# Kernel tuning notes

Hardware: AMD Instinct MI355X
Metric: run time of the kernel (lower is better)

Reference implementation:

```python
import jax, jax.numpy as jnp
import numpy as np

# Hyperparameters matching init_kwargs
IN_CH = 64
OUT_CH = 128
KERNEL = (3, 3)
STRIDE = (1, 1)
PADDING = 'SAME'
K_ORDER = 3          # spline order
G_INTERVALS = 3      # grid intervals
GRID_MIN, GRID_MAX = -1.0, 1.0
N_BASIS = G_INTERVALS + K_ORDER  # basis functions per input = 6
PATCH_DIM = IN_CH * KERNEL[0] * KERNEL[1]  # 576


def _grid():
    # Extended uniform knot vector: G + 2k + 1 knots
    h = (GRID_MAX - GRID_MIN) / G_INTERVALS
    return jnp.arange(-K_ORDER, G_INTERVALS + K_ORDER + 1, dtype=jnp.float32) * h + GRID_MIN


def _b_splines(x):
    # x: [N, n_in] -> bases: [N, n_in, G + k]
    grid = _grid()  # [G + 2k + 1]
    xe = x[..., None]  # [N, n_in, 1]
    bases = ((xe >= grid[:-1]) & (xe < grid[1:])).astype(x.dtype)  # order-0, [N, n_in, G+2k]
    for p in range(1, K_ORDER + 1):
        left = (xe - grid[: -(p + 1)]) / (grid[p:-1] - grid[: -(p + 1)]) * bases[..., :-1]
        right = (grid[p + 1:] - xe) / (grid[p + 1:] - grid[1:-p]) * bases[..., 1:]
        bases = left + right
    return bases  # [N, n_in, G + k]


def setup_inputs() -> dict:
    key = jax.random.key(0)
    k0, k1, k2, k3 = jax.random.split(key, 4)
    x = jax.random.normal(k0, (8, 64, 64, IN_CH), dtype=jnp.float32)
    base_w = jax.random.normal(k1, (OUT_CH, PATCH_DIM), dtype=jnp.float32) * 0.05
    spline_w = jax.random.normal(k2, (OUT_CH, PATCH_DIM, N_BASIS), dtype=jnp.float32) * 0.05
    bias = jax.random.normal(k3, (OUT_CH,), dtype=jnp.float32) * 0.05
    return {'x': x, 'base_w': base_w, 'spline_w': spline_w, 'bias': bias}


def reference(x, base_w, spline_w, bias):
    batch = x.shape[0]
    dn = ('NHWC', 'HWIO', 'NHWC')
    patches = jax.lax.conv_general_dilated_patches(
        lhs=x, filter_shape=KERNEL, window_strides=STRIDE, padding=PADDING,
        dimension_numbers=dn)  # [B, H, W, patch_dim]
    out_spatial = patches.shape[1:-1]
    p = patches.reshape(-1, PATCH_DIM)  # [N, patch_dim]
    # EfficientKAN: residual (silu) branch + spline branch + bias
    base_out = jax.nn.silu(p) @ base_w.T                      # [N, out]
    bases = _b_splines(p)                                      # [N, patch_dim, G+k]
    spline_out = jnp.einsum('nig,oig->no', bases, spline_w)    # [N, out]
    y = base_out + spline_out + bias
    return y.reshape(batch, *out_spatial, OUT_CH)
```

## Files before the change

kernel.cpp:

```cpp
#include <hip/hip_runtime.h>

typedef __attribute__((ext_vector_type(8))) short short8;
typedef __attribute__((ext_vector_type(16))) float f32x16;

#define FT2_SHORTS (512u * 4356u * 8u)
#define PLANE16    4356

typedef __attribute__((address_space(3))) unsigned int lds_u32_t;
typedef __attribute__((address_space(1))) const unsigned int g_u32_t;

__device__ __forceinline__ unsigned short f2bf(float x) {
    union { float f; unsigned u; } v; v.f = x;
    unsigned r = v.u + 0x7FFFu + ((v.u >> 16) & 1u);
    return (unsigned short)(r >> 16);
}

__device__ __forceinline__ void feat8(float p, unsigned short* uf) {
    float e   = __expf(-p);
    float sig = 1.f / (1.f + e);
    uf[0] = f2bf(p * sig);
    float u  = p * 1.5f + 4.5f;
    float fj = floorf(u);
    int   j0 = (int)fj;
    float t  = u - fj;
    bool  inr = (u >= 0.f) && (u < 9.f);
    float t2 = t * t, t3 = t2 * t;
    const float c16 = 1.f / 6.f;
    float r0 = t3 * c16;
    float r1 = (-3.f * t3 + 3.f * t2 + 3.f * t + 1.f) * c16;
    float r2 = (3.f * t3 - 6.f * t2 + 4.f) * c16;
    float s1 = 1.f - t;
    float r3 = s1 * s1 * s1 * c16;
#pragma unroll
    for (int g = 0; g < 6; ++g) {
        int r = j0 - g;
        float v = (r == 0) ? r0 : ((r == 1) ? r1 : ((r == 2) ? r2 : ((r == 3) ? r3 : 0.f)));
        uf[1 + g] = f2bf(inr ? v : 0.f);
    }
    uf[7] = 0;
}

__global__ __launch_bounds__(256)
void prep_all(const float* __restrict__ x,
              const float* __restrict__ bw, const float* __restrict__ sw,
              unsigned short* __restrict__ ft, unsigned short* __restrict__ wt) {
    const int blk = blockIdx.x;
    const int tid = threadIdx.x;

    if (tid < 144) {
        int idx = blk * 144 + tid;
        int o = idx / 576;
        int i = idx - o * 576;
        int slab = i >> 3, e = i & 7;
        union { unsigned short u[8]; uint4 v; } pk;
        pk.u[0] = f2bf(bw[o * 576 + i]);
        const float* s = sw + (size_t)(o * 576 + i) * 6;
#pragma unroll
        for (int f = 0; f < 6; ++f) pk.u[1 + f] = f2bf(s[f]);
        pk.u[7] = 0;
        *(uint4*)(wt + ((size_t)slab * 8192 + e * 1024 + o * 8)) = pk.v;
    }

    {
        short8 pad = { 0, 0, (short)0x3CAB, (short)0x3EF5,
                       (short)0x3EF5, (short)0x3CAB, 0, 0 };
        for (int t = tid; t < 260; t += 256) {
            int yy, xx;
            if (t < 66)       { yy = 0;       xx = t; }
            else if (t < 132) { yy = 65;      xx = t - 66; }
            else if (t < 196) { yy = t - 131; xx = 0; }
            else              { yy = t - 195; xx = 65; }
            ((short8*)ft)[blk * PLANE16 + yy * 66 + xx] = pad;
        }
    }

    __shared__ float Xl[64 * 65];
    const int b = blk >> 6, y = blk & 63;
    const float* xl = x + (size_t)blk * 4096;
    for (int f4 = tid; f4 < 1024; f4 += 256) {
        float4 v = ((const float4*)xl)[f4];
        int xx = f4 >> 4, c4 = (f4 & 15) << 2;
        float* d = &Xl[xx * 65 + c4];
        d[0] = v.x; d[1] = v.y; d[2] = v.z; d[3] = v.w;
    }
    __syncthreads();
    const int xx = tid & 63;
    const int cw = tid >> 6;
#pragma unroll 4
    for (int p = 0; p < 16; ++p) {
        int c = cw + (p << 2);
        float pv = Xl[xx * 65 + c];
        union { unsigned short u[8]; uint4 v; } pk;
        feat8(pv, pk.u);
        size_t o16 = (size_t)(c * 8 + b) * PLANE16 + (y + 1) * 66 + (xx + 1);
        *(uint4*)(ft + (o16 << 3)) = pk.v;
    }
}

#define BUF_SHORTS 16384

#define STAGE(sl, q_)                                                                 \
    {                                                                                 \
        unsigned short* bufq = Bufs + (q_) * BUF_SHORTS;                              \
        const unsigned short* bsrc = wt + (size_t)(sl) * 8192;                        \
        _Pragma("unroll")                                                             \
        for (int t = 0; t < 2; ++t) {                                                 \
            int u = wave * 2 + t;                     \
            if (u < 16) {                                                             \
                int boff = u * 512 + lane * 8;                                        \
                __builtin_amdgcn_global_load_lds((g_u32_t*)(bsrc + boff),             \
                                                 (lds_u32_t*)(bufq + boff), 16, 0, 0);\
            } else {                                                                  \
                int ua  = u - 16;                                 \
                int ia  = (sl) * 8 + (ua >> 1);                                       \
                int ln  = ua & 1;                                                     \
                int c_  = (ia * 7282) >> 16;                                          \
                int i9_ = ia - c_ * 9;                                                \
                int kh_ = (i9_ * 11) >> 5;                                            \
                int kw_ = i9_ - kh_ * 3;                                              \
                const unsigned short* asrc = ft +                                     \
                    (((size_t)(c_ * 8 + b) * PLANE16 + (y0 + ln + kh_) * 66 + kw_)    \
                     << 3) + lane * 8;                                                \
                unsigned short* adst = bufq + 8192 + ua * 512 + lane * 8;             \
                __builtin_amdgcn_global_load_lds((g_u32_t*)asrc, (lds_u32_t*)adst,    \
                                                 16, 0, 0);                           \
            }                                                                         \
        }                                                                             \
    }

#define COMPUTE(q_)                                                                   \
    {                                                                                 \
        const unsigned short* bufr = Bufs + (q_) * BUF_SHORTS;                        \
        const unsigned short* Ab = bufr + 8192 + ((iloc << 1) + mh) * 512;            \
        const unsigned short* Bb = bufr + iloc * 1024 + nh * 512;                     \
        short8 a0 = *(const short8*)(Ab + l32 * 8);                                   \
        short8 a1 = *(const short8*)(Ab + 256 + l32 * 8);                             \
        short8 b0 = *(const short8*)(Bb + l32 * 8);                                   \
        short8 b1 = *(const short8*)(Bb + 256 + l32 * 8);                             \
        acc00 = __builtin_amdgcn_mfma_f32_32x32x16_bf16(a0, b0, acc00, 0, 0, 0);      \
        acc01 = __builtin_amdgcn_mfma_f32_32x32x16_bf16(a0, b1, acc01, 0, 0, 0);      \
        acc10 = __builtin_amdgcn_mfma_f32_32x32x16_bf16(a1, b0, acc10, 0, 0, 0);      \
        acc11 = __builtin_amdgcn_mfma_f32_32x32x16_bf16(a1, b1, acc11, 0, 0, 0);      \
    }

#define PHASE(q_, n_, stagesl, dostage_)                                              \
    {                                                                                 \
        asm volatile("s_waitcnt vmcnt(" #n_ ")" ::: "memory");                        \
        __builtin_amdgcn_s_barrier();                                                 \
        asm volatile("" ::: "memory");                                                \
        __builtin_amdgcn_s_setprio(1);                                                \
        COMPUTE(q_)                                                                   \
        __builtin_amdgcn_s_setprio(0);                                                \
        asm volatile("" ::: "memory");                                                \
        __builtin_amdgcn_s_barrier();                                                 \
        asm volatile("" ::: "memory");                                                \
        if (dostage_) STAGE(stagesl, q_);                                             \
    }

#define DUMPA(base_, A_)                                                              \
    {   float4* s4 = (float4*)(red + (base_));                                        \
        _Pragma("unroll")                                                             \
        for (int c = 0; c < 4; ++c)                                                   \
            s4[c * 64 + lane] = make_float4(A_[4*c], A_[4*c+1], A_[4*c+2], A_[4*c+3]); }
#define ADDA(base_, A_)                                                               \
    {   const float4* s4 = (const float4*)(red + (base_));                            \
        _Pragma("unroll")                                                             \
        for (int c = 0; c < 4; ++c) {                                                 \
            float4 rv = s4[c * 64 + lane];                                            \
            A_[4*c] += rv.x; A_[4*c+1] += rv.y; A_[4*c+2] += rv.z; A_[4*c+3] += rv.w; } }

__global__ __launch_bounds__(1024, 4)
void convkan_gemm(const unsigned short* __restrict__ ft,
                  const unsigned short* __restrict__ wt,
                  const float* __restrict__ bias,
                  float* __restrict__ out) {
    extern __shared__ unsigned short Bufs[];

    const int tid  = threadIdx.x;
    const int mb   = blockIdx.x;
    const int lane = tid & 63;
    const int wave = tid >> 6;
    const int kq   = wave >> 2;
    const int mh   = (wave >> 1) & 1;
    const int nh   = wave & 1;
    const int l32  = lane & 31;
    const int h    = lane >> 5;
    const int iloc = (kq << 1) + h;

    const int b  = mb >> 5;
    const int y0 = (mb & 31) << 1;

    f32x16 acc00, acc01, acc10, acc11;
#pragma unroll
    for (int e = 0; e < 16; ++e) { acc00[e] = 0.f; acc01[e] = 0.f; acc10[e] = 0.f; acc11[e] = 0.f; }

    STAGE(0, 0);
    STAGE(1, 1);
    STAGE(2, 2);

    for (int it3 = 0; it3 < 23; ++it3) {
        const int it = it3 * 3;
        PHASE(0, 4, it + 3, true)
        PHASE(1, 4, it + 4, true)
        PHASE(2, 4, it + 5, true)
    }
    PHASE(0, 4, 0, false)
    PHASE(1, 2, 0, false)
    PHASE(2, 0, 0, false)

    __syncthreads();
    float* red = (float*)Bufs;
    const int grp = mh * 2 + nh;

    if (kq >= 2) { DUMPA(((grp << 1) + (kq - 2)) * 2048,        acc00);
                   DUMPA(((grp << 1) + (kq - 2)) * 2048 + 1024, acc01); }
    __syncthreads();
    if (kq < 2)  { ADDA(((grp << 1) + kq) * 2048,        acc00);
                   ADDA(((grp << 1) + kq) * 2048 + 1024, acc01); }
    __syncthreads();
    if (kq >= 2) { DUMPA(((grp << 1) + (kq - 2)) * 2048,        acc10);
                   DUMPA(((grp << 1) + (kq - 2)) * 2048 + 1024, acc11); }
    __syncthreads();
    if (kq < 2)  { ADDA(((grp << 1) + kq) * 2048,        acc10);
                   ADDA(((grp << 1) + kq) * 2048 + 1024, acc11); }
    __syncthreads();
    if (kq == 1) { DUMPA(grp * 4096,        acc00); DUMPA(grp * 4096 + 1024, acc01);
                   DUMPA(grp * 4096 + 2048, acc10); DUMPA(grp * 4096 + 3072, acc11); }
    __syncthreads();
    if (kq == 0) {
        ADDA(grp * 4096,        acc00); ADDA(grp * 4096 + 1024, acc01);
        ADDA(grp * 4096 + 2048, acc10); ADDA(grp * 4096 + 3072, acc11);

        const int ncol = nh * 64 + l32;
        const float bv0 = bias[ncol];
        const float bv1 = bias[ncol + 32];
        const int prow = mb * 128 + mh * 64;
#pragma unroll
        for (int r = 0; r < 16; ++r) {
            int mrow = (r & 3) + ((r >> 2) << 3) + 4 * h;
            float* p = out + (size_t)(prow + mrow) * 128 + ncol;
            p[0]  = acc00[r] + bv0;
            p[32] = acc01[r] + bv1;
            float* p2 = out + (size_t)(prow + 32 + mrow) * 128 + ncol;
            p2[0]  = acc10[r] + bv0;
            p2[32] = acc11[r] + bv1;
        }
    }
}

extern "C" void kernel_launch(void* const* d_in, const int* in_sizes, int n_in,
                              void* d_out, int out_size, void* d_ws, size_t ws_size,
                              hipStream_t stream) {
    (void)in_sizes; (void)n_in; (void)ws_size; (void)out_size;
    const float* x        = (const float*)d_in[0];
    const float* base_w   = (const float*)d_in[1];
    const float* spline_w = (const float*)d_in[2];
    const float* bias     = (const float*)d_in[3];
    float* out = (float*)d_out;

    unsigned short* ft = (unsigned short*)d_ws;
    unsigned short* wt = ft + FT2_SHORTS;

    hipLaunchKernelGGL(prep_all, dim3(512), dim3(256), 0, stream,
                       x, base_w, spline_w, ft, wt);

    const int shmem = 3 * BUF_SHORTS * 2;
    (void)hipFuncSetAttribute((const void*)convkan_gemm,
                              hipFuncAttributeMaxDynamicSharedMemorySize, shmem);
    hipLaunchKernelGGL(convkan_gemm, dim3(256), dim3(1024), shmem, stream,
                       ft, wt, bias, out);
}
```

Baseline: 133.4 us.

## Halve GEMM block tile to one output row and double grid with swizzled block order

```diff
diff --git a/kernel.cpp b/kernel.cpp
--- a/kernel.cpp
+++ b/kernel.cpp
@@ -97,31 +97,30 @@
     }
 }
 
-#define BUF_SHORTS 16384
+#define BUF_SHORTS 12288
 
 #define STAGE(sl, q_)                                                                 \
     {                                                                                 \
         unsigned short* bufq = Bufs + (q_) * BUF_SHORTS;                              \
         const unsigned short* bsrc = wt + (size_t)(sl) * 8192;                        \
         _Pragma("unroll")                                                             \
-        for (int t = 0; t < 2; ++t) {                                                 \
-            int u = wave * 2 + t;                     \
+        for (int t = 0; t < 3; ++t) {                                                 \
+            int u = wave * 3 + t;                     \
             if (u < 16) {                                                             \
                 int boff = u * 512 + lane * 8;                                        \
                 __builtin_amdgcn_global_load_lds((g_u32_t*)(bsrc + boff),             \
                                                  (lds_u32_t*)(bufq + boff), 16, 0, 0);\
             } else {                                                                  \
-                int ua  = u - 16;                                 \
-                int ia  = (sl) * 8 + (ua >> 1);                                       \
-                int ln  = ua & 1;                                                     \
+                int idx = u - 16;                                     \
+                int ia  = (sl) * 8 + idx;                                             \
                 int c_  = (ia * 7282) >> 16;                                          \
                 int i9_ = ia - c_ * 9;                                                \
                 int kh_ = (i9_ * 11) >> 5;                                            \
                 int kw_ = i9_ - kh_ * 3;                                              \
                 const unsigned short* asrc = ft +                                     \
-                    (((size_t)(c_ * 8 + b) * PLANE16 + (y0 + ln + kh_) * 66 + kw_)    \
-                     << 3) + lane * 8;                                                \
-                unsigned short* adst = bufq + 8192 + ua * 512 + lane * 8;             \
+                    (((size_t)(c_ * 8 + b) * PLANE16 + (y + kh_) * 66 + kw_) << 3)    \
+                    + lane * 8;                                                       \
+                unsigned short* adst = bufq + 8192 + idx * 512 + lane * 8;            \
                 __builtin_amdgcn_global_load_lds((g_u32_t*)asrc, (lds_u32_t*)adst,    \
                                                  16, 0, 0);                           \
             }                                                                         \
@@ -131,10 +130,10 @@
 #define COMPUTE(q_)                                                                   \
     {                                                                                 \
         const unsigned short* bufr = Bufs + (q_) * BUF_SHORTS;                        \
-        const unsigned short* Ab = bufr + 8192 + ((iloc << 1) + mh) * 512;            \
+        const unsigned short* Ab = bufr + 8192 + iloc * 512;                          \
         const unsigned short* Bb = bufr + iloc * 1024 + nh * 512;                     \
         short8 a0 = *(const short8*)(Ab + l32 * 8);                                   \
-        short8 a1 = *(const short8*)(Ab + 256 + l32 * 8);                             \
+        short8 a1 = *(const short8*)(Ab + (32 + l32) * 8);                            \
         short8 b0 = *(const short8*)(Bb + l32 * 8);                                   \
         short8 b1 = *(const short8*)(Bb + 256 + l32 * 8);                             \
         acc00 = __builtin_amdgcn_mfma_f32_32x32x16_bf16(a0, b0, acc00, 0, 0, 0);      \
@@ -169,7 +168,7 @@
             float4 rv = s4[c * 64 + lane];                                            \
             A_[4*c] += rv.x; A_[4*c+1] += rv.y; A_[4*c+2] += rv.z; A_[4*c+3] += rv.w; } }
 
-__global__ __launch_bounds__(1024, 4)
+__global__ __launch_bounds__(512, 4)
 void convkan_gemm(const unsigned short* __restrict__ ft,
                   const unsigned short* __restrict__ wt,
                   const float* __restrict__ bias,
@@ -177,18 +176,18 @@
     extern __shared__ unsigned short Bufs[];
 
     const int tid  = threadIdx.x;
-    const int mb   = blockIdx.x;
+    const int blk  = blockIdx.x;
+    const int mb   = ((blk & 7) << 6) | (blk >> 3);
     const int lane = tid & 63;
     const int wave = tid >> 6;
-    const int kq   = wave >> 2;
-    const int mh   = (wave >> 1) & 1;
+    const int kq   = wave >> 1;
     const int nh   = wave & 1;
     const int l32  = lane & 31;
     const int h    = lane >> 5;
     const int iloc = (kq << 1) + h;
 
-    const int b  = mb >> 5;
-    const int y0 = (mb & 31) << 1;
+    const int b = mb >> 6;
+    const int y = mb & 63;
 
     f32x16 acc00, acc01, acc10, acc11;
 #pragma unroll
@@ -200,41 +199,40 @@
 
     for (int it3 = 0; it3 < 23; ++it3) {
         const int it = it3 * 3;
-        PHASE(0, 4, it + 3, true)
-        PHASE(1, 4, it + 4, true)
-        PHASE(2, 4, it + 5, true)
-    }
-    PHASE(0, 4, 0, false)
-    PHASE(1, 2, 0, false)
+        PHASE(0, 6, it + 3, true)
+        PHASE(1, 6, it + 4, true)
+        PHASE(2, 6, it + 5, true)
+    }
+    PHASE(0, 6, 0, false)
+    PHASE(1, 3, 0, false)
     PHASE(2, 0, 0, false)
 
     __syncthreads();
     float* red = (float*)Bufs;
-    const int grp = mh * 2 + nh;
-
-    if (kq >= 2) { DUMPA(((grp << 1) + (kq - 2)) * 2048,        acc00);
-                   DUMPA(((grp << 1) + (kq - 2)) * 2048 + 1024, acc01); }
-    __syncthreads();
-    if (kq < 2)  { ADDA(((grp << 1) + kq) * 2048,        acc00);
-                   ADDA(((grp << 1) + kq) * 2048 + 1024, acc01); }
-    __syncthreads();
-    if (kq >= 2) { DUMPA(((grp << 1) + (kq - 2)) * 2048,        acc10);
-                   DUMPA(((grp << 1) + (kq - 2)) * 2048 + 1024, acc11); }
-    __syncthreads();
-    if (kq < 2)  { ADDA(((grp << 1) + kq) * 2048,        acc10);
-                   ADDA(((grp << 1) + kq) * 2048 + 1024, acc11); }
-    __syncthreads();
-    if (kq == 1) { DUMPA(grp * 4096,        acc00); DUMPA(grp * 4096 + 1024, acc01);
-                   DUMPA(grp * 4096 + 2048, acc10); DUMPA(grp * 4096 + 3072, acc11); }
+
+    if (kq >= 2) { DUMPA(((nh << 1) + (kq - 2)) * 2048,        acc00);
+                   DUMPA(((nh << 1) + (kq - 2)) * 2048 + 1024, acc01); }
+    __syncthreads();
+    if (kq < 2)  { ADDA(((nh << 1) + kq) * 2048,        acc00);
+                   ADDA(((nh << 1) + kq) * 2048 + 1024, acc01); }
+    __syncthreads();
+    if (kq >= 2) { DUMPA(((nh << 1) + (kq - 2)) * 2048,        acc10);
+                   DUMPA(((nh << 1) + (kq - 2)) * 2048 + 1024, acc11); }
+    __syncthreads();
+    if (kq < 2)  { ADDA(((nh << 1) + kq) * 2048,        acc10);
+                   ADDA(((nh << 1) + kq) * 2048 + 1024, acc11); }
+    __syncthreads();
+    if (kq == 1) { DUMPA(nh * 4096,        acc00); DUMPA(nh * 4096 + 1024, acc01);
+                   DUMPA(nh * 4096 + 2048, acc10); DUMPA(nh * 4096 + 3072, acc11); }
     __syncthreads();
     if (kq == 0) {
-        ADDA(grp * 4096,        acc00); ADDA(grp * 4096 + 1024, acc01);
-        ADDA(grp * 4096 + 2048, acc10); ADDA(grp * 4096 + 3072, acc11);
+        ADDA(nh * 4096,        acc00); ADDA(nh * 4096 + 1024, acc01);
+        ADDA(nh * 4096 + 2048, acc10); ADDA(nh * 4096 + 3072, acc11);
 
         const int ncol = nh * 64 + l32;
         const float bv0 = bias[ncol];
         const float bv1 = bias[ncol + 32];
-        const int prow = mb * 128 + mh * 64;
+        const int prow = mb * 64;
 #pragma unroll
         for (int r = 0; r < 16; ++r) {
             int mrow = (r & 3) + ((r >> 2) << 3) + 4 * h;
@@ -267,6 +265,6 @@
     const int shmem = 3 * BUF_SHORTS * 2;
     (void)hipFuncSetAttribute((const void*)convkan_gemm,
                               hipFuncAttributeMaxDynamicSharedMemorySize, shmem);
-    hipLaunchKernelGGL(convkan_gemm, dim3(256), dim3(1024), shmem, stream,
+    hipLaunchKernelGGL(convkan_gemm, dim3(512), dim3(512), shmem, stream,
                        ft, wt, bias, out);
 }
```

New measurement: 135.7 us. About the same (+1.8%).

## Split K across two blocks with atomic accumulation and swizzled block order

Applied to the files above, without the earlier changes.

```diff
diff --git a/kernel.cpp b/kernel.cpp
--- a/kernel.cpp
+++ b/kernel.cpp
@@ -97,22 +97,22 @@
     }
 }
 
-#define BUF_SHORTS 16384
-
-#define STAGE(sl, q_)                                                                 \
+#define BUF_SHORTS 8192
+
+#define STAGE(hs, q_)                                                                 \
     {                                                                                 \
         unsigned short* bufq = Bufs + (q_) * BUF_SHORTS;                              \
-        const unsigned short* bsrc = wt + (size_t)(sl) * 8192;                        \
+        const unsigned short* bsrc = wt + (size_t)(kk72 + (hs)) * 4096;               \
         _Pragma("unroll")                                                             \
         for (int t = 0; t < 2; ++t) {                                                 \
-            int u = wave * 2 + t;                     \
-            if (u < 16) {                                                             \
+            int u = wave * 2 + t;                       \
+            if (u < 8) {                                                              \
                 int boff = u * 512 + lane * 8;                                        \
                 __builtin_amdgcn_global_load_lds((g_u32_t*)(bsrc + boff),             \
                                                  (lds_u32_t*)(bufq + boff), 16, 0, 0);\
             } else {                                                                  \
-                int ua  = u - 16;                                 \
-                int ia  = (sl) * 8 + (ua >> 1);                                       \
+                int ua  = u - 8;                              \
+                int ia  = (kk72 + (hs)) * 4 + (ua >> 1);                              \
                 int ln  = ua & 1;                                                     \
                 int c_  = (ia * 7282) >> 16;                                          \
                 int i9_ = ia - c_ * 9;                                                \
@@ -121,7 +121,7 @@
                 const unsigned short* asrc = ft +                                     \
                     (((size_t)(c_ * 8 + b) * PLANE16 + (y0 + ln + kh_) * 66 + kw_)    \
                      << 3) + lane * 8;                                                \
-                unsigned short* adst = bufq + 8192 + ua * 512 + lane * 8;             \
+                unsigned short* adst = bufq + 4096 + ua * 512 + lane * 8;             \
                 __builtin_amdgcn_global_load_lds((g_u32_t*)asrc, (lds_u32_t*)adst,    \
                                                  16, 0, 0);                           \
             }                                                                         \
@@ -131,19 +131,17 @@
 #define COMPUTE(q_)                                                                   \
     {                                                                                 \
         const unsigned short* bufr = Bufs + (q_) * BUF_SHORTS;                        \
-        const unsigned short* Ab = bufr + 8192 + ((iloc << 1) + mh) * 512;            \
-        const unsigned short* Bb = bufr + iloc * 1024 + nh * 512;                     \
-        short8 a0 = *(const short8*)(Ab + l32 * 8);                                   \
-        short8 a1 = *(const short8*)(Ab + 256 + l32 * 8);                             \
-        short8 b0 = *(const short8*)(Bb + l32 * 8);                                   \
-        short8 b1 = *(const short8*)(Bb + 256 + l32 * 8);                             \
+        short8 a0 = *(const short8*)(bufr + aoff);                                    \
+        short8 a1 = *(const short8*)(bufr + aoff + 256);                              \
+        short8 b0 = *(const short8*)(bufr + boff);                                    \
+        short8 b1 = *(const short8*)(bufr + boff + 256);                              \
         acc00 = __builtin_amdgcn_mfma_f32_32x32x16_bf16(a0, b0, acc00, 0, 0, 0);      \
         acc01 = __builtin_amdgcn_mfma_f32_32x32x16_bf16(a0, b1, acc01, 0, 0, 0);      \
         acc10 = __builtin_amdgcn_mfma_f32_32x32x16_bf16(a1, b0, acc10, 0, 0, 0);      \
         acc11 = __builtin_amdgcn_mfma_f32_32x32x16_bf16(a1, b1, acc11, 0, 0, 0);      \
     }
 
-#define PHASE(q_, n_, stagesl, dostage_)                                              \
+#define PHASE(q_, n_, stagehs, dostage_)                                              \
     {                                                                                 \
         asm volatile("s_waitcnt vmcnt(" #n_ ")" ::: "memory");                        \
         __builtin_amdgcn_s_barrier();                                                 \
@@ -154,7 +152,7 @@
         asm volatile("" ::: "memory");                                                \
         __builtin_amdgcn_s_barrier();                                                 \
         asm volatile("" ::: "memory");                                                \
-        if (dostage_) STAGE(stagesl, q_);                                             \
+        if (dostage_) STAGE(stagehs, q_);                                             \
     }
 
 #define DUMPA(base_, A_)                                                              \
@@ -169,7 +167,7 @@
             float4 rv = s4[c * 64 + lane];                                            \
             A_[4*c] += rv.x; A_[4*c+1] += rv.y; A_[4*c+2] += rv.z; A_[4*c+3] += rv.w; } }
 
-__global__ __launch_bounds__(1024, 4)
+__global__ __launch_bounds__(512, 4)
 void convkan_gemm(const unsigned short* __restrict__ ft,
                   const unsigned short* __restrict__ wt,
                   const float* __restrict__ bias,
@@ -177,7 +175,10 @@
     extern __shared__ unsigned short Bufs[];
 
     const int tid  = threadIdx.x;
-    const int mb   = blockIdx.x;
+    const int blk  = blockIdx.x;
+    const int kk   = blk >> 8;
+    const int mbr  = blk & 255;
+    const int mb   = ((mbr & 7) << 5) | (mbr >> 3);
     const int lane = tid & 63;
     const int wave = tid >> 6;
     const int kq   = wave >> 2;
@@ -185,10 +186,14 @@
     const int nh   = wave & 1;
     const int l32  = lane & 31;
     const int h    = lane >> 5;
-    const int iloc = (kq << 1) + h;
 
     const int b  = mb >> 5;
     const int y0 = (mb & 31) << 1;
+    const int kk72 = kk * 72;
+
+    const int eloc = (kq << 1) + h;
+    const int aoff = 4096 + eloc * 1024 + mh * 512 + l32 * 8;
+    const int boff = eloc * 1024 + nh * 512 + l32 * 8;
 
     f32x16 acc00, acc01, acc10, acc11;
 #pragma unroll
@@ -212,38 +217,32 @@
     float* red = (float*)Bufs;
     const int grp = mh * 2 + nh;
 
-    if (kq >= 2) { DUMPA(((grp << 1) + (kq - 2)) * 2048,        acc00);
-                   DUMPA(((grp << 1) + (kq - 2)) * 2048 + 1024, acc01); }
-    __syncthreads();
-    if (kq < 2)  { ADDA(((grp << 1) + kq) * 2048,        acc00);
-                   ADDA(((grp << 1) + kq) * 2048 + 1024, acc01); }
-    __syncthreads();
-    if (kq >= 2) { DUMPA(((grp << 1) + (kq - 2)) * 2048,        acc10);
-                   DUMPA(((grp << 1) + (kq - 2)) * 2048 + 1024, acc11); }
-    __syncthreads();
-    if (kq < 2)  { ADDA(((grp << 1) + kq) * 2048,        acc10);
-                   ADDA(((grp << 1) + kq) * 2048 + 1024, acc11); }
-    __syncthreads();
-    if (kq == 1) { DUMPA(grp * 4096,        acc00); DUMPA(grp * 4096 + 1024, acc01);
-                   DUMPA(grp * 4096 + 2048, acc10); DUMPA(grp * 4096 + 3072, acc11); }
+    if (kq == 1) { DUMPA(grp * 2048,        acc00);
+                   DUMPA(grp * 2048 + 1024, acc01); }
+    __syncthreads();
+    if (kq == 0) { ADDA(grp * 2048,        acc00);
+                   ADDA(grp * 2048 + 1024, acc01); }
+    __syncthreads();
+    if (kq == 1) { DUMPA(grp * 2048,        acc10);
+                   DUMPA(grp * 2048 + 1024, acc11); }
     __syncthreads();
     if (kq == 0) {
-        ADDA(grp * 4096,        acc00); ADDA(grp * 4096 + 1024, acc01);
-        ADDA(grp * 4096 + 2048, acc10); ADDA(grp * 4096 + 3072, acc11);
+        ADDA(grp * 2048,        acc10);
+        ADDA(grp * 2048 + 1024, acc11);
 
         const int ncol = nh * 64 + l32;
-        const float bv0 = bias[ncol];
-        const float bv1 = bias[ncol + 32];
+        const float bv0 = kk ? 0.f : bias[ncol];
+        const float bv1 = kk ? 0.f : bias[ncol + 32];
         const int prow = mb * 128 + mh * 64;
 #pragma unroll
         for (int r = 0; r < 16; ++r) {
             int mrow = (r & 3) + ((r >> 2) << 3) + 4 * h;
             float* p = out + (size_t)(prow + mrow) * 128 + ncol;
-            p[0]  = acc00[r] + bv0;
-            p[32] = acc01[r] + bv1;
+            atomicAdd(p,      acc00[r] + bv0);
+            atomicAdd(p + 32, acc01[r] + bv1);
             float* p2 = out + (size_t)(prow + 32 + mrow) * 128 + ncol;
-            p2[0]  = acc10[r] + bv0;
-            p2[32] = acc11[r] + bv1;
+            atomicAdd(p2,      acc10[r] + bv0);
+            atomicAdd(p2 + 32, acc11[r] + bv1);
         }
     }
 }
@@ -251,7 +250,7 @@
 extern "C" void kernel_launch(void* const* d_in, const int* in_sizes, int n_in,
                               void* d_out, int out_size, void* d_ws, size_t ws_size,
                               hipStream_t stream) {
-    (void)in_sizes; (void)n_in; (void)ws_size; (void)out_size;
+    (void)in_sizes; (void)n_in; (void)ws_size;
     const float* x        = (const float*)d_in[0];
     const float* base_w   = (const float*)d_in[1];
     const float* spline_w = (const float*)d_in[2];
@@ -261,12 +260,13 @@
     unsigned short* ft = (unsigned short*)d_ws;
     unsigned short* wt = ft + FT2_SHORTS;
 
+    hipMemsetAsync(out, 0, (size_t)out_size * sizeof(float), stream);
     hipLaunchKernelGGL(prep_all, dim3(512), dim3(256), 0, stream,
                        x, base_w, spline_w, ft, wt);
 
     const int shmem = 3 * BUF_SHORTS * 2;
     (void)hipFuncSetAttribute((const void*)convkan_gemm,
                               hipFuncAttributeMaxDynamicSharedMemorySize, shmem);
-    hipLaunchKernelGGL(convkan_gemm, dim3(256), dim3(1024), shmem, stream,
+    hipLaunchKernelGGL(convkan_gemm, dim3(512), dim3(512), shmem, stream,
                        ft, wt, bias, out);
 }
```

Measured after the change: 150.5 us. 1.13x slower.

## Load GEMM operands directly from global into registers, dropping LDS staging

Applied to the files above, without the earlier changes.

```diff
diff --git a/kernel.cpp b/kernel.cpp
--- a/kernel.cpp
+++ b/kernel.cpp
@@ -5,9 +5,6 @@
 
 #define FT2_SHORTS (512u * 4356u * 8u)
 #define PLANE16    4356
-
-typedef __attribute__((address_space(3))) unsigned int lds_u32_t;
-typedef __attribute__((address_space(1))) const unsigned int g_u32_t;
 
 __device__ __forceinline__ unsigned short f2bf(float x) {
     union { float f; unsigned u; } v; v.f = x;
@@ -51,14 +48,13 @@
         int idx = blk * 144 + tid;
         int o = idx / 576;
         int i = idx - o * 576;
-        int slab = i >> 3, e = i & 7;
         union { unsigned short u[8]; uint4 v; } pk;
         pk.u[0] = f2bf(bw[o * 576 + i]);
         const float* s = sw + (size_t)(o * 576 + i) * 6;
 #pragma unroll
         for (int f = 0; f < 6; ++f) pk.u[1 + f] = f2bf(s[f]);
         pk.u[7] = 0;
-        *(uint4*)(wt + ((size_t)slab * 8192 + e * 1024 + o * 8)) = pk.v;
+        *(uint4*)(wt + ((size_t)i * 1024 + o * 8)) = pk.v;
     }
 
     {
@@ -97,64 +93,38 @@
     }
 }
 
-#define BUF_SHORTS 16384
-
-#define STAGE(sl, q_)                                                                 \
-    {                                                                                 \
-        unsigned short* bufq = Bufs + (q_) * BUF_SHORTS;                              \
-        const unsigned short* bsrc = wt + (size_t)(sl) * 8192;                        \
-        _Pragma("unroll")                                                             \
-        for (int t = 0; t < 2; ++t) {                                                 \
-            int u = wave * 2 + t;                     \
-            if (u < 16) {                                                             \
-                int boff = u * 512 + lane * 8;                                        \
-                __builtin_amdgcn_global_load_lds((g_u32_t*)(bsrc + boff),             \
-                                                 (lds_u32_t*)(bufq + boff), 16, 0, 0);\
-            } else {                                                                  \
-                int ua  = u - 16;                                 \
-                int ia  = (sl) * 8 + (ua >> 1);                                       \
-                int ln  = ua & 1;                                                     \
-                int c_  = (ia * 7282) >> 16;                                          \
-                int i9_ = ia - c_ * 9;                                                \
-                int kh_ = (i9_ * 11) >> 5;                                            \
-                int kw_ = i9_ - kh_ * 3;                                              \
-                const unsigned short* asrc = ft +                                     \
-                    (((size_t)(c_ * 8 + b) * PLANE16 + (y0 + ln + kh_) * 66 + kw_)    \
-                     << 3) + lane * 8;                                                \
-                unsigned short* adst = bufq + 8192 + ua * 512 + lane * 8;             \
-                __builtin_amdgcn_global_load_lds((g_u32_t*)asrc, (lds_u32_t*)adst,    \
-                                                 16, 0, 0);                           \
-            }                                                                         \
-        }                                                                             \
-    }
-
-#define COMPUTE(q_)                                                                   \
-    {                                                                                 \
-        const unsigned short* bufr = Bufs + (q_) * BUF_SHORTS;                        \
-        const unsigned short* Ab = bufr + 8192 + ((iloc << 1) + mh) * 512;            \
-        const unsigned short* Bb = bufr + iloc * 1024 + nh * 512;                     \
-        short8 a0 = *(const short8*)(Ab + l32 * 8);                                   \
-        short8 a1 = *(const short8*)(Ab + 256 + l32 * 8);                             \
-        short8 b0 = *(const short8*)(Bb + l32 * 8);                                   \
-        short8 b1 = *(const short8*)(Bb + 256 + l32 * 8);                             \
-        acc00 = __builtin_amdgcn_mfma_f32_32x32x16_bf16(a0, b0, acc00, 0, 0, 0);      \
-        acc01 = __builtin_amdgcn_mfma_f32_32x32x16_bf16(a0, b1, acc01, 0, 0, 0);      \
-        acc10 = __builtin_amdgcn_mfma_f32_32x32x16_bf16(a1, b0, acc10, 0, 0, 0);      \
-        acc11 = __builtin_amdgcn_mfma_f32_32x32x16_bf16(a1, b1, acc11, 0, 0, 0);      \
-    }
-
-#define PHASE(q_, n_, stagesl, dostage_)                                              \
-    {                                                                                 \
-        asm volatile("s_waitcnt vmcnt(" #n_ ")" ::: "memory");                        \
-        __builtin_amdgcn_s_barrier();                                                 \
-        asm volatile("" ::: "memory");                                                \
-        __builtin_amdgcn_s_setprio(1);                                                \
-        COMPUTE(q_)                                                                   \
-        __builtin_amdgcn_s_setprio(0);                                                \
-        asm volatile("" ::: "memory");                                                \
-        __builtin_amdgcn_s_barrier();                                                 \
-        asm volatile("" ::: "memory");                                                \
-        if (dostage_) STAGE(stagesl, q_);                                             \
+#define DZU 4460544u
+
+#define MFMA4(P)                                                                      \
+    acc00 = __builtin_amdgcn_mfma_f32_32x32x16_bf16(P##a0, P##b0, acc00, 0, 0, 0);    \
+    acc01 = __builtin_amdgcn_mfma_f32_32x32x16_bf16(P##a0, P##b1, acc01, 0, 0, 0);    \
+    acc10 = __builtin_amdgcn_mfma_f32_32x32x16_bf16(P##a1, P##b0, acc10, 0, 0, 0);    \
+    acc11 = __builtin_amdgcn_mfma_f32_32x32x16_bf16(P##a1, P##b1, acc11, 0, 0, 0);
+
+#define ISS(P, CAX, S2)                                                               \
+    P##a0 = *(const short8*)(ftc + (CAX) + aoff##S2);                                 \
+    P##a1 = *(const short8*)(ftc + (CAX) + aoff##S2 + 512);                           \
+    P##b0 = *(const short8*)(wtc + bv);                                               \
+    P##b1 = *(const short8*)(wtc + bv + 512);                                         \
+    bv += 4096u;
+
+#define PAIR(SA, SB, CAX, CAN, LAST)                                                  \
+    MFMA4(SA) ISS(SA, CAX, 2)                                                         \
+    MFMA4(SB) ISS(SB, CAX, 3)                                                         \
+    MFMA4(SA) ISS(SA, CAX, 4)                                                         \
+    MFMA4(SB) ISS(SB, CAX, 5)                                                         \
+    MFMA4(SA) ISS(SA, CAX, 6)                                                         \
+    MFMA4(SB) ISS(SB, CAX, 7)                                                         \
+    MFMA4(SA) ISS(SA, CAX, 8)                                                         \
+    bv += 110592u;                       \
+    MFMA4(SB) if (!(LAST)) { ISS(SB, CAN, 0) }                                        \
+    MFMA4(SA) if (!(LAST)) { ISS(SA, CAN, 1) }
+
+#define MKAOFF(S)                                                                     \
+    int aoff##S; {                                                                    \
+        int t_ = 2 * (S) + h; int co_ = (t_ >= 9) ? 1 : 0; int j_ = t_ - 9 * co_;     \
+        int kh_ = (j_ * 11) >> 5; int kw_ = j_ - kh_ * 3;                             \
+        aoff##S = co_ * (8 * PLANE16 * 16) + (kh_ * 66 + kw_) * 16;                   \
     }
 
 #define DUMPA(base_, A_)                                                              \
@@ -174,10 +144,11 @@
                   const unsigned short* __restrict__ wt,
                   const float* __restrict__ bias,
                   float* __restrict__ out) {
-    extern __shared__ unsigned short Bufs[];
+    __shared__ float red[16384];
 
     const int tid  = threadIdx.x;
-    const int mb   = blockIdx.x;
+    const int blk  = blockIdx.x;
+    const int mb   = ((blk & 7) << 5) | (blk >> 3);
     const int lane = tid & 63;
     const int wave = tid >> 6;
     const int kq   = wave >> 2;
@@ -185,31 +156,38 @@
     const int nh   = wave & 1;
     const int l32  = lane & 31;
     const int h    = lane >> 5;
-    const int iloc = (kq << 1) + h;
 
     const int b  = mb >> 5;
     const int y0 = (mb & 31) << 1;
 
+    const char* ftc = (const char*)ft;
+    const char* wtc = (const char*)wt;
+
+    MKAOFF(0) MKAOFF(1) MKAOFF(2) MKAOFF(3) MKAOFF(4)
+    MKAOFF(5) MKAOFF(6) MKAOFF(7) MKAOFF(8)
+
+    unsigned cax = ((unsigned)((16 * kq + b) * PLANE16 + (y0 + mh) * 66 + l32)) << 4;
+    unsigned can = cax + DZU;
+    unsigned bv  = ((unsigned)(18 * kq + h) << 11) + (((unsigned)(nh * 64 + l32)) << 4);
+
     f32x16 acc00, acc01, acc10, acc11;
 #pragma unroll
     for (int e = 0; e < 16; ++e) { acc00[e] = 0.f; acc01[e] = 0.f; acc10[e] = 0.f; acc11[e] = 0.f; }
 
-    STAGE(0, 0);
-    STAGE(1, 1);
-    STAGE(2, 2);
-
-    for (int it3 = 0; it3 < 23; ++it3) {
-        const int it = it3 * 3;
-        PHASE(0, 4, it + 3, true)
-        PHASE(1, 4, it + 4, true)
-        PHASE(2, 4, it + 5, true)
-    }
-    PHASE(0, 4, 0, false)
-    PHASE(1, 2, 0, false)
-    PHASE(2, 0, 0, false)
-
-    __syncthreads();
-    float* red = (float*)Bufs;
+    short8 Aa0, Aa1, Ab0, Ab1;
+    short8 Ba0, Ba1, Bb0, Bb1;
+
+    ISS(A, cax, 0)
+    ISS(B, cax, 1)
+
+    for (int w = 0; w < 3; ++w) {
+        PAIR(A, B, cax, can, 0) cax = can; can += DZU;
+        PAIR(B, A, cax, can, 0) cax = can; can += DZU;
+    }
+    PAIR(A, B, cax, can, 0) cax = can;
+    PAIR(B, A, cax, cax, 1)
+
+    __syncthreads();
     const int grp = mh * 2 + nh;
 
     if (kq >= 2) { DUMPA(((grp << 1) + (kq - 2)) * 2048,        acc00);
@@ -264,9 +242,6 @@
     hipLaunchKernelGGL(prep_all, dim3(512), dim3(256), 0, stream,
                        x, base_w, spline_w, ft, wt);
 
-    const int shmem = 3 * BUF_SHORTS * 2;
-    (void)hipFuncSetAttribute((const void*)convkan_gemm,
-                              hipFuncAttributeMaxDynamicSharedMemorySize, shmem);
-    hipLaunchKernelGGL(convkan_gemm, dim3(256), dim3(1024), shmem, stream,
+    hipLaunchKernelGGL(convkan_gemm, dim3(256), dim3(1024), 0, stream,
                        ft, wt, bias, out);
 }
```

After: 269.9 us. 2.02x slower.
